# Optimization experiments

Measured on AMD Instinct MI355X. Metric: run time of the kernel, lower is better.

The kernel has to match this reference:

```python
import jax, jax.numpy as jnp
import numpy as np

H, HKV, D = 16, 4, 64
ROPE_BASE = 10000.0
EPS = 1e-6


def _rms_norm(x):
    return x * jax.lax.rsqrt(jnp.mean(x * x, axis=-1, keepdims=True) + EPS)


def _rope_cos_sin(T, dtype):
    inv_freq = 1.0 / (ROPE_BASE ** (jnp.arange(0, D, 2, dtype=jnp.float32) / D))  # [D/2]
    t = jnp.arange(T, dtype=jnp.float32)
    freqs = jnp.outer(t, inv_freq)  # [T, D/2]
    return jnp.cos(freqs)[None, :, None, :].astype(dtype), jnp.sin(freqs)[None, :, None, :].astype(dtype)


def _apply_rope(x, cos, sin):
    d = x.shape[-1] // 2
    x1, x2 = x[..., :d], x[..., d:]
    return jnp.concatenate([x1 * cos + x2 * sin, -x1 * sin + x2 * cos], axis=-1)


def setup_inputs() -> dict:
    key = jax.random.key(0)
    ks = jax.random.split(key, 6)
    B, T, dm = 1, 2048, 1024
    x = jax.random.normal(ks[0], (B, T, dm), dtype=jnp.float32)
    q_w = jax.random.normal(ks[1], (H * D, dm), dtype=jnp.float32) * 0.02
    k_w = jax.random.normal(ks[2], (HKV * D, dm), dtype=jnp.float32) * 0.02
    v_w = jax.random.normal(ks[3], (HKV * D, dm), dtype=jnp.float32) * 0.02
    o_w = jax.random.normal(ks[4], (dm, H * D), dtype=jnp.float32) * 0.02
    temp = jnp.ones((H,), dtype=jnp.float32) * np.sqrt(D)  # per-head temperature buffer
    curvature = jnp.asarray(1.0, dtype=jnp.float32)
    return {"x": x, "q_w": q_w, "k_w": k_w, "v_w": v_w, "o_w": o_w, "temp": temp, "curvature": curvature}


def reference(x, q_w, k_w, v_w, o_w, temp, curvature):
    B, T, dm = x.shape
    # projections
    q = (x @ q_w.T).reshape(B, T, H, D)
    k = (x @ k_w.T).reshape(B, T, HKV, D)
    v = (x @ v_w.T).reshape(B, T, HKV, D)
    q, k = _rms_norm(q), _rms_norm(k)
    cos, sin = _rope_cos_sin(T, q.dtype)
    q = _apply_rope(q, cos, sin)
    k = _apply_rope(k, cos, sin)
    # GQA: repeat kv heads
    rep = H // HKV
    k = jnp.repeat(k, rep, axis=2)  # [B,T,H,D]
    v = jnp.repeat(v, rep, axis=2)
    c = curvature
    # hyperboloid lift: time component x0 = sqrt(1/c + ||x||^2)
    q0 = jnp.sqrt(1.0 / c + jnp.sum(q * q, axis=-1))  # [B,T,H]
    k0 = jnp.sqrt(1.0 / c + jnp.sum(k * k, axis=-1))
    # Minkowski inner product <q,k>_L = q.k_spatial - q0*k0  -> [B,H,Tq,Tk]
    mink = jnp.einsum('bqhd,bkhd->bhqk', q, k) - q0.transpose(0, 2, 1)[..., :, None] * k0.transpose(0, 2, 1)[..., None, :]
    # Lorentz distance d = arccosh(clamp(-c*<q,k>_L, 1+eps)) / sqrt(c)
    dist = jnp.arccosh(jnp.maximum(-c * mink, 1.0 + 1e-5)) / jnp.sqrt(c)
    scores = -dist / temp[None, :, None, None]
    causal = jnp.tril(jnp.ones((T, T), dtype=bool))
    scores = jnp.where(causal[None, None], scores, -jnp.inf)
    w = jax.nn.softmax(scores, axis=-1)  # [B,H,Tq,Tk]
    attn = jnp.einsum('bhqk,bkhd->bqhd', w, v).reshape(B, T, H * D)
    out = attn @ o_w.T  # [B,T,dm]
    spatial_norm = jnp.mean(jnp.sqrt(jnp.sum(q * q, axis=-1)))
    return out, spatial_norm
```

## Files before the change

kernel.cpp:

```cpp
#include <hip/hip_runtime.h>
#include <hip/hip_bf16.h>

typedef __attribute__((ext_vector_type(8))) short short8;
typedef __attribute__((ext_vector_type(4))) short bf16x4;
typedef __attribute__((ext_vector_type(4))) float f32x4;

#define TT 2048
#define DM 1024
#define NH 16
#define NKV 4
#define HD 64

#define MFMA32(a,b,c) __builtin_amdgcn_mfma_f32_16x16x32_bf16(a,b,c,0,0,0)
#define MFMA16(a,b,c) __builtin_amdgcn_mfma_f32_16x16x16bf16_1k(a,b,c,0,0,0)

__device__ __forceinline__ unsigned short f2bf(float x){
  unsigned int u = __float_as_uint(x);
  u += 0x7fffu + ((u >> 16) & 1u);
  return (unsigned short)(u >> 16);
}
__device__ __forceinline__ unsigned int pkbf2(float x, float y){
  union { __hip_bfloat162 h; unsigned int u; } t;
  t.h = __float22bfloat162_rn(make_float2(x, y));
  return t.u;
}
__device__ __forceinline__ void gl_lds16(const unsigned short* g, unsigned short* l){
  __builtin_amdgcn_global_load_lds(
      (__attribute__((address_space(1))) void*)g,
      (__attribute__((address_space(3))) void*)l, 16, 0, 0);
}

__global__ __launch_bounds__(256) void convertw_kernel(
    const float* __restrict__ x,
    const float* __restrict__ qw, const float* __restrict__ kw,
    const float* __restrict__ vw, const float* __restrict__ ow,
    unsigned short* __restrict__ xb,
    unsigned short* __restrict__ wqkv, unsigned short* __restrict__ owb){
  long v = (long)blockIdx.x * 256 + threadIdx.x;
  const float* src; unsigned short* dst; long base;
  if      (v < 524288) { src = x;  dst = xb;             base = v; }
  else if (v < 786432) { src = qw; dst = wqkv;           base = v - 524288; }
  else if (v < 851968) { src = kw; dst = wqkv + 1048576; base = v - 786432; }
  else if (v < 917504) { src = vw; dst = wqkv + 1310720; base = v - 851968; }
  else                 { src = ow; dst = owb;            base = v - 917504; }
  f32x4 d = *(const f32x4*)(src + base * 4);
  uint2 pk = { pkbf2(d[0], d[1]), pkbf2(d[2], d[3]) };
  *(uint2*)(dst + base * 4) = pk;
}

__global__ __launch_bounds__(256) void gemm1_fused(
    const unsigned short* __restrict__ xb, const unsigned short* __restrict__ wqkv,
    unsigned short* __restrict__ qb, unsigned short* __restrict__ kb,
    unsigned short* __restrict__ vt,
    float* __restrict__ q0, float* __restrict__ k0,
    float* __restrict__ bpart, const float* __restrict__ curv){
  __shared__ __align__(16) unsigned short As[4 * 128 * 32];
  __shared__ __align__(16) unsigned short Bs[4 * 64 * 32];
  __shared__ float bsum;
  const int tid = threadIdx.x, lane = tid & 63, wave = tid >> 6;
  const int hIdx = blockIdx.x;
  const int bm = blockIdx.y * 128, bn = hIdx * 64;
  const int ml = lane & 15, quad = lane >> 4;
  if (tid == 0) bsum = 0.f;
  f32x4 acc[2][4];
  const f32x4 z = {0.f, 0.f, 0.f, 0.f};
#pragma unroll
  for (int i = 0; i < 2; i++)
#pragma unroll
    for (int j = 0; j < 4; j++) acc[i][j] = z;

  const int srow = tid >> 2, scol = (tid & 3) * 8;
  const unsigned short* Ag0 = xb   + (long)(bm + srow) * 1024 + scol;
  const unsigned short* Ag1 = Ag0 + 64 * 1024;
  const unsigned short* Bg  = wqkv + (long)(bn + srow) * 1024 + scol;

  for (int kk = 0; kk < 1024; kk += 128){
    __syncthreads();
#pragma unroll
    for (int half = 0; half < 4; half++){
      gl_lds16(Ag0 + kk + half * 32, As + half * 4096 + wave * 512);
      gl_lds16(Ag1 + kk + half * 32, As + half * 4096 + 2048 + wave * 512);
      gl_lds16(Bg  + kk + half * 32, Bs + half * 2048 + wave * 512);
    }
    __syncthreads();
#pragma unroll
    for (int half = 0; half < 4; half++){
      const unsigned short* Ah = As + half * 4096;
      const unsigned short* Bh = Bs + half * 2048;
      short8 a0 = *(const short8*)&Ah[(wave * 32 + ml) * 32 + quad * 8];
      short8 a1 = *(const short8*)&Ah[(wave * 32 + 16 + ml) * 32 + quad * 8];
      short8 b0 = *(const short8*)&Bh[(ml) * 32 + quad * 8];
      short8 b1 = *(const short8*)&Bh[(16 + ml) * 32 + quad * 8];
      short8 b2 = *(const short8*)&Bh[(32 + ml) * 32 + quad * 8];
      short8 b3 = *(const short8*)&Bh[(48 + ml) * 32 + quad * 8];
      acc[0][0] = MFMA32(a0, b0, acc[0][0]);
      acc[0][1] = MFMA32(a0, b1, acc[0][1]);
      acc[0][2] = MFMA32(a0, b2, acc[0][2]);
      acc[0][3] = MFMA32(a0, b3, acc[0][3]);
      acc[1][0] = MFMA32(a1, b0, acc[1][0]);
      acc[1][1] = MFMA32(a1, b1, acc[1][1]);
      acc[1][2] = MFMA32(a1, b2, acc[1][2]);
      acc[1][3] = MFMA32(a1, b3, acc[1][3]);
    }
  }

  if (hIdx < 20){
    const bool isq = hIdx < 16;
    const int h = isq ? hIdx : hIdx - 16;
    const float c = curv[0];
    unsigned short* ob = isq ? qb : kb;
    float* o0p = isq ? q0 : k0;
    const float if0 = __builtin_amdgcn_exp2f((float)ml        * (-13.287712379549449f / 32.f));
    const float if1 = __builtin_amdgcn_exp2f((float)(16 + ml) * (-13.287712379549449f / 32.f));
    float bl = 0.f;
#pragma unroll
    for (int i = 0; i < 2; i++){
#pragma unroll
      for (int r = 0; r < 4; r++){
        const int t = bm + wave * 32 + i * 16 + quad * 4 + r;
        float v0 = acc[i][0][r], v1 = acc[i][1][r], v2 = acc[i][2][r], v3 = acc[i][3][r];
        float ss = v0 * v0 + v1 * v1 + v2 * v2 + v3 * v3;
        ss += __shfl_xor(ss, 1); ss += __shfl_xor(ss, 2);
        ss += __shfl_xor(ss, 4); ss += __shfl_xor(ss, 8);
        float scale = __builtin_amdgcn_rsqf(ss * (1.f / 64.f) + 1e-6f);
        float x0 = v0 * scale, x1 = v1 * scale, x2 = v2 * scale, x3 = v3 * scale;
        float sn0, cs0, sn1, cs1;
        __sincosf((float)t * if0, &sn0, &cs0);
        __sincosf((float)t * if1, &sn1, &cs1);
        unsigned short* op = ob + ((long)h * TT + t) * 64;
        op[ml]      = f2bf( x0 * cs0 + x2 * sn0);
        op[16 + ml] = f2bf( x1 * cs1 + x3 * sn1);
        op[32 + ml] = f2bf( x2 * cs0 - x0 * sn0);
        op[48 + ml] = f2bf( x3 * cs1 - x1 * sn1);
        if (ml == 0){
          float sq = ss * scale * scale;
          o0p[h * TT + t] = __builtin_amdgcn_sqrtf(1.f / c + sq);
          if (isq) bl += __builtin_amdgcn_sqrtf(sq);
        }
      }
    }
    if (isq && ml == 0) atomicAdd(&bsum, bl);
  } else {
    const int hk = hIdx - 20;
#pragma unroll
    for (int i = 0; i < 2; i++){
      const int tile = (bm >> 4) + wave * 2 + i;
#pragma unroll
      for (int j = 0; j < 4; j++){
        uint2 w2 = { pkbf2(acc[i][j][0], acc[i][j][1]), pkbf2(acc[i][j][2], acc[i][j][3]) };
        unsigned short* dst = vt + ((long)(hk * 128 + tile) * 64 + j * 16 + ml) * 16 + quad * 4;
        *(uint2*)dst = w2;
      }
    }
  }
  __syncthreads();
  if (tid == 0) bpart[blockIdx.y * 24 + hIdx] = bsum;
}

__global__ __launch_bounds__(256, 3) void attn_kernel(
    const unsigned short* __restrict__ qb_, const unsigned short* __restrict__ kb_,
    const unsigned short* __restrict__ vt_,
    const float* __restrict__ q0_, const float* __restrict__ k0_,
    const float* __restrict__ temp, const float* __restrict__ curv,
    unsigned short* __restrict__ attn_out,
    const float* __restrict__ bpart, float* __restrict__ out_scalar){
  __shared__ float lds[8 * 1104];
  const int tid = threadIdx.x, lane = tid & 63, wave = tid >> 6;
  const int qt  = 127 - (blockIdx.x >> 3);
  const int sub = blockIdx.x & 7;
  const int kvh = sub >> 1, hp = sub & 1;
  const int h0 = kvh * 4 + hp * 2, h1 = h0 + 1;
  const int i0 = qt * 16;
  const int ml = lane & 15, quad = lane >> 4;
  const float c = curv[0];
  const float rsc = __builtin_amdgcn_rsqf(c);
  const float fac0 = -rsc / temp[h0];
  const float fac1 = -rsc / temp[h1];
  const f32x4 z = {0.f, 0.f, 0.f, 0.f};
  const unsigned short* kh = kb_ + (long)kvh * TT * 64;
  const unsigned short* vh = vt_ + (long)kvh * 128 * 1024;
  const float* k0h = k0_ + kvh * TT;

  short8 qa0 = *(const short8*)&qb_[((long)h0 * TT + i0 + ml) * 64 + quad * 8];
  short8 qa1 = *(const short8*)&qb_[((long)h0 * TT + i0 + ml) * 64 + 32 + quad * 8];
  short8 qb0 = *(const short8*)&qb_[((long)h1 * TT + i0 + ml) * 64 + quad * 8];
  short8 qb1 = *(const short8*)&qb_[((long)h1 * TT + i0 + ml) * 64 + 32 + quad * 8];
  const float q0c0 = c * q0_[h0 * TT + i0 + ml];
  const float q0c1 = c * q0_[h1 * TT + i0 + ml];
  const int rowq = i0 + ml;

  f32x4 o0[4], o1[4];
#pragma unroll
  for (int dt = 0; dt < 4; dt++){ o0[dt] = z; o1[dt] = z; }
  float l0 = 0.f, l1 = 0.f;

  const int nt = (i0 + 47) >> 5;

#pragma unroll 1
  for (int t = wave; t < nt; t += 4){
    const int j0 = t << 5;
    const unsigned short* kp = kh + (long)j0 * 64;
    short8 ka0 = *(const short8*)(kp + ml * 64 + quad * 8);
    short8 ka1 = *(const short8*)(kp + ml * 64 + 32 + quad * 8);
    short8 kc0 = *(const short8*)(kp + (16 + ml) * 64 + quad * 8);
    short8 kc1 = *(const short8*)(kp + (16 + ml) * 64 + 32 + quad * 8);
    f32x4 k0a = *(const f32x4*)(k0h + j0 + quad * 4);
    f32x4 k0b = *(const f32x4*)(k0h + j0 + 16 + quad * 4);
    const unsigned short* vpa = vh + (long)(j0 >> 4) * 1024;
    bf16x4 vfa0 = *(const bf16x4*)(vpa + ( 0 + ml) * 16 + quad * 4);
    bf16x4 vfa1 = *(const bf16x4*)(vpa + (16 + ml) * 16 + quad * 4);
    bf16x4 vfa2 = *(const bf16x4*)(vpa + (32 + ml) * 16 + quad * 4);
    bf16x4 vfa3 = *(const bf16x4*)(vpa + (48 + ml) * 16 + quad * 4);
    bf16x4 vfb0 = *(const bf16x4*)(vpa + 1024 + ( 0 + ml) * 16 + quad * 4);
    bf16x4 vfb1 = *(const bf16x4*)(vpa + 1024 + (16 + ml) * 16 + quad * 4);
    bf16x4 vfb2 = *(const bf16x4*)(vpa + 1024 + (32 + ml) * 16 + quad * 4);
    bf16x4 vfb3 = *(const bf16x4*)(vpa + 1024 + (48 + ml) * 16 + quad * 4);

    const int keyb = j0 + quad * 4;
    const bool nm = (j0 + 31 > i0);
    {
      f32x4 s0 = z, s1 = z;
      s0 = MFMA32(ka0, qa0, s0);
      s0 = MFMA32(ka1, qa1, s0);
      s1 = MFMA32(kc0, qa0, s1);
      s1 = MFMA32(kc1, qa1, s1);
      float p0[4], p1[4];
#pragma unroll
      for (int r = 0; r < 4; r++){
        float argA = fmaxf(__builtin_fmaf(-c, s0[r], q0c0 * k0a[r]), 1.00001f);
        float wA   = argA + __builtin_amdgcn_sqrtf(__builtin_fmaf(argA, argA, -1.f));
        float pA   = __builtin_amdgcn_exp2f(fac0 * __builtin_amdgcn_logf(wA));
        float argB = fmaxf(__builtin_fmaf(-c, s1[r], q0c0 * k0b[r]), 1.00001f);
        float wB   = argB + __builtin_amdgcn_sqrtf(__builtin_fmaf(argB, argB, -1.f));
        float pB   = __builtin_amdgcn_exp2f(fac0 * __builtin_amdgcn_logf(wB));
        if (nm){
          if (keyb + r > rowq)      pA = 0.f;
          if (keyb + 16 + r > rowq) pB = 0.f;
        }
        p0[r] = pA; p1[r] = pB;
        l0 += pA + pB;
      }
      uint2 pua = { pkbf2(p0[0], p0[1]), pkbf2(p0[2], p0[3]) };
      uint2 pub = { pkbf2(p1[0], p1[1]), pkbf2(p1[2], p1[3]) };
      bf16x4 pfa = *(bf16x4*)&pua;
      bf16x4 pfb = *(bf16x4*)&pub;
      o0[0] = MFMA16(vfa0, pfa, o0[0]);
      o0[1] = MFMA16(vfa1, pfa, o0[1]);
      o0[2] = MFMA16(vfa2, pfa, o0[2]);
      o0[3] = MFMA16(vfa3, pfa, o0[3]);
      o0[0] = MFMA16(vfb0, pfb, o0[0]);
      o0[1] = MFMA16(vfb1, pfb, o0[1]);
      o0[2] = MFMA16(vfb2, pfb, o0[2]);
      o0[3] = MFMA16(vfb3, pfb, o0[3]);
    }
    {
      f32x4 s0 = z, s1 = z;
      s0 = MFMA32(ka0, qb0, s0);
      s0 = MFMA32(ka1, qb1, s0);
      s1 = MFMA32(kc0, qb0, s1);
      s1 = MFMA32(kc1, qb1, s1);
      float p0[4], p1[4];
#pragma unroll
      for (int r = 0; r < 4; r++){
        float argA = fmaxf(__builtin_fmaf(-c, s0[r], q0c1 * k0a[r]), 1.00001f);
        float wA   = argA + __builtin_amdgcn_sqrtf(__builtin_fmaf(argA, argA, -1.f));
        float pA   = __builtin_amdgcn_exp2f(fac1 * __builtin_amdgcn_logf(wA));
        float argB = fmaxf(__builtin_fmaf(-c, s1[r], q0c1 * k0b[r]), 1.00001f);
        float wB   = argB + __builtin_amdgcn_sqrtf(__builtin_fmaf(argB, argB, -1.f));
        float pB   = __builtin_amdgcn_exp2f(fac1 * __builtin_amdgcn_logf(wB));
        if (nm){
          if (keyb + r > rowq)      pA = 0.f;
          if (keyb + 16 + r > rowq) pB = 0.f;
        }
        p0[r] = pA; p1[r] = pB;
        l1 += pA + pB;
      }
      uint2 pua = { pkbf2(p0[0], p0[1]), pkbf2(p0[2], p0[3]) };
      uint2 pub = { pkbf2(p1[0], p1[1]), pkbf2(p1[2], p1[3]) };
      bf16x4 pfa = *(bf16x4*)&pua;
      bf16x4 pfb = *(bf16x4*)&pub;
      o1[0] = MFMA16(vfa0, pfa, o1[0]);
      o1[1] = MFMA16(vfa1, pfa, o1[1]);
      o1[2] = MFMA16(vfa2, pfa, o1[2]);
      o1[3] = MFMA16(vfa3, pfa, o1[3]);
      o1[0] = MFMA16(vfb0, pfb, o1[0]);
      o1[1] = MFMA16(vfb1, pfb, o1[1]);
      o1[2] = MFMA16(vfb2, pfb, o1[2]);
      o1[3] = MFMA16(vfb3, pfb, o1[3]);
    }
  }
  l0 += __shfl_xor(l0, 16); l0 += __shfl_xor(l0, 32);
  l1 += __shfl_xor(l1, 16); l1 += __shfl_xor(l1, 32);
  {
    float* w0 = lds + wave * 1104;
    float* w1 = lds + (4 + wave) * 1104;
#pragma unroll
    for (int dt = 0; dt < 4; dt++){
      *(f32x4*)&w0[ml * 68 + dt * 16 + quad * 4] = o0[dt];
      *(f32x4*)&w1[ml * 68 + dt * 16 + quad * 4] = o1[dt];
    }
    if (quad == 0){ w0[1088 + ml] = l0; w1[1088 + ml] = l1; }
  }
  __syncthreads();
  {
    const int row = tid >> 4, c0 = (tid & 15) * 4;
#pragma unroll 1
    for (int hb = 0; hb < 2; hb++){
      const float* base = lds + hb * 4 * 1104;
      float L = 0.f; f32x4 s = z;
#pragma unroll
      for (int w = 0; w < 4; w++){
        const float* rg = base + w * 1104;
        L += rg[1088 + row];
        f32x4 t2 = *(const f32x4*)&rg[row * 68 + c0];
        s[0] += t2[0]; s[1] += t2[1]; s[2] += t2[2]; s[3] += t2[3];
      }
      float invL = __builtin_amdgcn_rcpf(L);
      const int h = hb ? h1 : h0;
      uint2 o = { pkbf2(s[0] * invL, s[1] * invL), pkbf2(s[2] * invL, s[3] * invL) };
      *(uint2*)&attn_out[(long)(i0 + row) * 1024 + h * 64 + c0] = o;
    }
  }
  if (blockIdx.x == 0 && tid < 64){
    float s = 0.f;
    for (int i = lane; i < 384; i += 64) s += bpart[i];
#pragma unroll
    for (int off = 1; off < 64; off <<= 1) s += __shfl_xor(s, off);
    if (lane == 0) out_scalar[0] = s * (1.f / 32768.f);
  }
}

__global__ __launch_bounds__(256) void gemm2_kernel(
    const unsigned short* __restrict__ A, const unsigned short* __restrict__ B,
    float* __restrict__ C){
  __shared__ __align__(16) unsigned short As[2 * 8192];
  __shared__ __align__(16) unsigned short Bs[2 * 4096];
  const int tid = threadIdx.x, lane = tid & 63, wave = tid >> 6;
  const int bm = blockIdx.y * 128, bn = blockIdx.x * 64;
  const int ml = lane & 15, quad = lane >> 4;
  f32x4 acc[2][4];
  const f32x4 z = {0.f, 0.f, 0.f, 0.f};
#pragma unroll
  for (int i = 0; i < 2; i++)
#pragma unroll
    for (int j = 0; j < 4; j++) acc[i][j] = z;

  const int srow = tid >> 2, scol = (tid & 3) * 8;
  const unsigned short* Ag0 = A + (long)(bm + srow) * 1024 + scol;
  const unsigned short* Ag1 = Ag0 + 64 * 1024;
  const unsigned short* Bg  = B + (long)(bn + srow) * 1024 + scol;

#define G2_STAGE(nb, ko)                                                  \
  do {                                                                    \
    gl_lds16(Ag0 + (ko),      As + (nb) * 8192 + wave * 512);             \
    gl_lds16(Ag1 + (ko),      As + (nb) * 8192 + 2048 + wave * 512);      \
    gl_lds16(Ag0 + (ko) + 32, As + (nb) * 8192 + 4096 + wave * 512);      \
    gl_lds16(Ag1 + (ko) + 32, As + (nb) * 8192 + 4096 + 2048 + wave * 512);\
    gl_lds16(Bg  + (ko),      Bs + (nb) * 4096 + wave * 512);             \
    gl_lds16(Bg  + (ko) + 32, Bs + (nb) * 4096 + 2048 + wave * 512);      \
  } while (0)

#define G2_COMPUTE(b)                                                     \
  do {                                                                    \
    _Pragma("unroll")                                                     \
    for (int half = 0; half < 2; half++){                                 \
      const unsigned short* Ah = As + (b) * 8192 + half * 4096;           \
      const unsigned short* Bh = Bs + (b) * 4096 + half * 2048;           \
      short8 a0 = *(const short8*)&Ah[(wave * 32 + ml) * 32 + quad * 8];  \
      short8 a1 = *(const short8*)&Ah[(wave * 32 + 16 + ml) * 32 + quad * 8];\
      short8 b0 = *(const short8*)&Bh[(ml) * 32 + quad * 8];              \
      short8 b1 = *(const short8*)&Bh[(16 + ml) * 32 + quad * 8];         \
      short8 b2 = *(const short8*)&Bh[(32 + ml) * 32 + quad * 8];         \
      short8 b3 = *(const short8*)&Bh[(48 + ml) * 32 + quad * 8];         \
      acc[0][0] = MFMA32(a0, b0, acc[0][0]);                              \
      acc[0][1] = MFMA32(a0, b1, acc[0][1]);                              \
      acc[0][2] = MFMA32(a0, b2, acc[0][2]);                              \
      acc[0][3] = MFMA32(a0, b3, acc[0][3]);                              \
      acc[1][0] = MFMA32(a1, b0, acc[1][0]);                              \
      acc[1][1] = MFMA32(a1, b1, acc[1][1]);                              \
      acc[1][2] = MFMA32(a1, b2, acc[1][2]);                              \
      acc[1][3] = MFMA32(a1, b3, acc[1][3]);                              \
    }                                                                     \
  } while (0)

  G2_STAGE(0, 0);
  __syncthreads();
  for (int kk = 0; kk < 1024; kk += 128){
    G2_STAGE(1, kk + 64);
    G2_COMPUTE(0);
    __syncthreads();
    if (kk + 128 < 1024) G2_STAGE(0, kk + 128);
    G2_COMPUTE(1);
    __syncthreads();
  }
#undef G2_STAGE
#undef G2_COMPUTE

#pragma unroll
  for (int i = 0; i < 2; i++)
#pragma unroll
    for (int j = 0; j < 4; j++)
#pragma unroll
      for (int r = 0; r < 4; r++)
        C[(long)(bm + wave * 32 + i * 16 + quad * 4 + r) * 1024 + bn + j * 16 + ml] = acc[i][j][r];
}

extern "C" void kernel_launch(void* const* d_in, const int* in_sizes, int n_in,
                              void* d_out, int out_size, void* d_ws, size_t ws_size,
                              hipStream_t stream){
  const float* x    = (const float*)d_in[0];
  const float* qw   = (const float*)d_in[1];
  const float* kw   = (const float*)d_in[2];
  const float* vw   = (const float*)d_in[3];
  const float* ow   = (const float*)d_in[4];
  const float* temp = (const float*)d_in[5];
  const float* curv = (const float*)d_in[6];
  float* out = (float*)d_out;

  char* ws = (char*)d_ws;
  size_t off = 0;
  auto alloc = [&](size_t bytes) -> char* {
    char* p = ws + off;
    off += (bytes + 255) & ~(size_t)255;
    return p;
  };
  unsigned short* xb   = (unsigned short*)alloc((size_t)TT * DM * 2);
  unsigned short* wqkv = (unsigned short*)alloc((size_t)1536 * DM * 2);
  unsigned short* owb  = (unsigned short*)alloc((size_t)DM * DM * 2);
  unsigned short* qb   = (unsigned short*)alloc((size_t)NH * TT * HD * 2);
  unsigned short* kb   = (unsigned short*)alloc((size_t)NKV * TT * HD * 2);
  unsigned short* vt   = (unsigned short*)alloc((size_t)NKV * TT * HD * 2);
  float*          q0   = (float*)alloc((size_t)NH * TT * 4);
  float*          k0   = (float*)alloc((size_t)NKV * TT * 4);
  unsigned short* attn = (unsigned short*)alloc((size_t)TT * DM * 2);
  float*          bpart= (float*)alloc((size_t)768 * 4);

  convertw_kernel<<<4608, 256, 0, stream>>>(x, qw, kw, vw, ow, xb, wqkv, owb);
  gemm1_fused<<<dim3(24, 16), 256, 0, stream>>>(xb, wqkv, qb, kb, vt, q0, k0, bpart, curv);
  attn_kernel<<<1024, 256, 0, stream>>>(qb, kb, vt, q0, k0, temp, curv, attn,
                                        bpart, out + (size_t)TT * DM);
  gemm2_kernel<<<dim3(16, 16), 256, 0, stream>>>(attn, owb, out);
}
```

Before: 140.3 us.

## Double query tile per attention block to reuse K/V loads across 32 rows

The attention kernel now processes 32 query rows per block instead of 16, with each wave computing four head/row-half combinations per key tile. Each loaded K and V fragment is therefore reused twice as often, cutting global/L2 traffic for K/V, and the grid is halved to 512 blocks. In exchange, register pressure roughly doubles, so launch bounds drop from 3 to 2 blocks per SM. Fewer blocks and coarser causal granularity may also worsen load balance and add wasted masked work on the diagonal tiles.

```diff
diff --git a/kernel.cpp b/kernel.cpp
--- a/kernel.cpp
+++ b/kernel.cpp
@@ -157,7 +157,44 @@
   if (tid == 0) bpart[blockIdx.y * 24 + hIdx] = bsum;
 }
 
-__global__ __launch_bounds__(256, 3) void attn_kernel(
+#define ATTN_STEP(QLO, QHI, Q0C, FAC, RQ, NM, OA, LACC)                         \
+  do {                                                                          \
+    f32x4 s0 = z, s1 = z;                                                       \
+    s0 = MFMA32(ka0, QLO, s0);                                                  \
+    s0 = MFMA32(ka1, QHI, s0);                                                  \
+    s1 = MFMA32(kc0, QLO, s1);                                                  \
+    s1 = MFMA32(kc1, QHI, s1);                                                  \
+    float p0[4], p1[4];                                                         \
+    _Pragma("unroll")                                                           \
+    for (int r = 0; r < 4; r++){                                                \
+      float argA = fmaxf(__builtin_fmaf(-c, s0[r], (Q0C) * k0a[r]), 1.00001f);  \
+      float wA   = argA + __builtin_amdgcn_sqrtf(__builtin_fmaf(argA, argA, -1.f)); \
+      float pA   = __builtin_amdgcn_exp2f((FAC) * __builtin_amdgcn_logf(wA));   \
+      float argB = fmaxf(__builtin_fmaf(-c, s1[r], (Q0C) * k0b[r]), 1.00001f);  \
+      float wB   = argB + __builtin_amdgcn_sqrtf(__builtin_fmaf(argB, argB, -1.f)); \
+      float pB   = __builtin_amdgcn_exp2f((FAC) * __builtin_amdgcn_logf(wB));   \
+      if (NM){                                                                  \
+        if (keyb + r > (RQ))      pA = 0.f;                                     \
+        if (keyb + 16 + r > (RQ)) pB = 0.f;                                     \
+      }                                                                         \
+      p0[r] = pA; p1[r] = pB;                                                   \
+      LACC += pA + pB;                                                          \
+    }                                                                           \
+    uint2 pua = { pkbf2(p0[0], p0[1]), pkbf2(p0[2], p0[3]) };                   \
+    uint2 pub = { pkbf2(p1[0], p1[1]), pkbf2(p1[2], p1[3]) };                   \
+    bf16x4 pfa = *(bf16x4*)&pua;                                                \
+    bf16x4 pfb = *(bf16x4*)&pub;                                                \
+    OA[0] = MFMA16(vfa0, pfa, OA[0]);                                           \
+    OA[1] = MFMA16(vfa1, pfa, OA[1]);                                           \
+    OA[2] = MFMA16(vfa2, pfa, OA[2]);                                           \
+    OA[3] = MFMA16(vfa3, pfa, OA[3]);                                           \
+    OA[0] = MFMA16(vfb0, pfb, OA[0]);                                           \
+    OA[1] = MFMA16(vfb1, pfb, OA[1]);                                           \
+    OA[2] = MFMA16(vfb2, pfb, OA[2]);                                           \
+    OA[3] = MFMA16(vfb3, pfb, OA[3]);                                           \
+  } while (0)
+
+__global__ __launch_bounds__(256, 2) void attn_kernel(
     const unsigned short* __restrict__ qb_, const unsigned short* __restrict__ kb_,
     const unsigned short* __restrict__ vt_,
     const float* __restrict__ q0_, const float* __restrict__ k0_,
@@ -166,11 +203,11 @@
     const float* __restrict__ bpart, float* __restrict__ out_scalar){
   __shared__ float lds[8 * 1104];
   const int tid = threadIdx.x, lane = tid & 63, wave = tid >> 6;
-  const int qt  = 127 - (blockIdx.x >> 3);
+  const int qt  = 63 - (blockIdx.x >> 3);
   const int sub = blockIdx.x & 7;
   const int kvh = sub >> 1, hp = sub & 1;
   const int h0 = kvh * 4 + hp * 2, h1 = h0 + 1;
-  const int i0 = qt * 16;
+  const int i0 = qt * 32;
   const int ml = lane & 15, quad = lane >> 4;
   const float c = curv[0];
   const float rsc = __builtin_amdgcn_rsqf(c);
@@ -181,20 +218,26 @@
   const unsigned short* vh = vt_ + (long)kvh * 128 * 1024;
   const float* k0h = k0_ + kvh * TT;
 
-  short8 qa0 = *(const short8*)&qb_[((long)h0 * TT + i0 + ml) * 64 + quad * 8];
-  short8 qa1 = *(const short8*)&qb_[((long)h0 * TT + i0 + ml) * 64 + 32 + quad * 8];
-  short8 qb0 = *(const short8*)&qb_[((long)h1 * TT + i0 + ml) * 64 + quad * 8];
-  short8 qb1 = *(const short8*)&qb_[((long)h1 * TT + i0 + ml) * 64 + 32 + quad * 8];
-  const float q0c0 = c * q0_[h0 * TT + i0 + ml];
-  const float q0c1 = c * q0_[h1 * TT + i0 + ml];
-  const int rowq = i0 + ml;
-
-  f32x4 o0[4], o1[4];
-#pragma unroll
-  for (int dt = 0; dt < 4; dt++){ o0[dt] = z; o1[dt] = z; }
-  float l0 = 0.f, l1 = 0.f;
-
-  const int nt = (i0 + 47) >> 5;
+  short8 qa00 = *(const short8*)&qb_[((long)h0 * TT + i0 + ml) * 64 + quad * 8];
+  short8 qa01 = *(const short8*)&qb_[((long)h0 * TT + i0 + ml) * 64 + 32 + quad * 8];
+  short8 qa10 = *(const short8*)&qb_[((long)h0 * TT + i0 + 16 + ml) * 64 + quad * 8];
+  short8 qa11 = *(const short8*)&qb_[((long)h0 * TT + i0 + 16 + ml) * 64 + 32 + quad * 8];
+  short8 qb00 = *(const short8*)&qb_[((long)h1 * TT + i0 + ml) * 64 + quad * 8];
+  short8 qb01 = *(const short8*)&qb_[((long)h1 * TT + i0 + ml) * 64 + 32 + quad * 8];
+  short8 qb10 = *(const short8*)&qb_[((long)h1 * TT + i0 + 16 + ml) * 64 + quad * 8];
+  short8 qb11 = *(const short8*)&qb_[((long)h1 * TT + i0 + 16 + ml) * 64 + 32 + quad * 8];
+  const float q0c0a = c * q0_[h0 * TT + i0 + ml];
+  const float q0c0b = c * q0_[h0 * TT + i0 + 16 + ml];
+  const float q0c1a = c * q0_[h1 * TT + i0 + ml];
+  const float q0c1b = c * q0_[h1 * TT + i0 + 16 + ml];
+  const int rqa = i0 + ml, rqb = i0 + 16 + ml;
+
+  f32x4 o0a[4], o0b[4], o1a[4], o1b[4];
+#pragma unroll
+  for (int dt = 0; dt < 4; dt++){ o0a[dt] = z; o0b[dt] = z; o1a[dt] = z; o1b[dt] = z; }
+  float l0a = 0.f, l0b = 0.f, l1a = 0.f, l1b = 0.f;
+
+  const int nt = (i0 + 63) >> 5;
 
 #pragma unroll 1
   for (int t = wave; t < nt; t += 4){
@@ -217,109 +260,55 @@
     bf16x4 vfb3 = *(const bf16x4*)(vpa + 1024 + (48 + ml) * 16 + quad * 4);
 
     const int keyb = j0 + quad * 4;
-    const bool nm = (j0 + 31 > i0);
+    const bool nma = (j0 + 31 > i0);
+    const bool nmb = (j0 + 31 > i0 + 16);
+
+    ATTN_STEP(qa00, qa01, q0c0a, fac0, rqa, nma, o0a, l0a);
+    ATTN_STEP(qa10, qa11, q0c0b, fac0, rqb, nmb, o0b, l0b);
+    ATTN_STEP(qb00, qb01, q0c1a, fac1, rqa, nma, o1a, l1a);
+    ATTN_STEP(qb10, qb11, q0c1b, fac1, rqb, nmb, o1b, l1b);
+  }
+  l0a += __shfl_xor(l0a, 16); l0a += __shfl_xor(l0a, 32);
+  l0b += __shfl_xor(l0b, 16); l0b += __shfl_xor(l0b, 32);
+  l1a += __shfl_xor(l1a, 16); l1a += __shfl_xor(l1a, 32);
+  l1b += __shfl_xor(l1b, 16); l1b += __shfl_xor(l1b, 32);
+
+#pragma unroll 1
+  for (int qs = 0; qs < 2; qs++){
     {
-      f32x4 s0 = z, s1 = z;
-      s0 = MFMA32(ka0, qa0, s0);
-      s0 = MFMA32(ka1, qa1, s0);
-      s1 = MFMA32(kc0, qa0, s1);
-      s1 = MFMA32(kc1, qa1, s1);
-      float p0[4], p1[4];
-#pragma unroll
-      for (int r = 0; r < 4; r++){
-        float argA = fmaxf(__builtin_fmaf(-c, s0[r], q0c0 * k0a[r]), 1.00001f);
-        float wA   = argA + __builtin_amdgcn_sqrtf(__builtin_fmaf(argA, argA, -1.f));
-        float pA   = __builtin_amdgcn_exp2f(fac0 * __builtin_amdgcn_logf(wA));
-        float argB = fmaxf(__builtin_fmaf(-c, s1[r], q0c0 * k0b[r]), 1.00001f);
-        float wB   = argB + __builtin_amdgcn_sqrtf(__builtin_fmaf(argB, argB, -1.f));
-        float pB   = __builtin_amdgcn_exp2f(fac0 * __builtin_amdgcn_logf(wB));
-        if (nm){
-          if (keyb + r > rowq)      pA = 0.f;
-          if (keyb + 16 + r > rowq) pB = 0.f;
+      float* w0 = lds + wave * 1104;
+      float* w1 = lds + (4 + wave) * 1104;
+#pragma unroll
+      for (int dt = 0; dt < 4; dt++){
+        *(f32x4*)&w0[ml * 68 + dt * 16 + quad * 4] = qs ? o0b[dt] : o0a[dt];
+        *(f32x4*)&w1[ml * 68 + dt * 16 + quad * 4] = qs ? o1b[dt] : o1a[dt];
+      }
+      if (quad == 0){
+        w0[1088 + ml] = qs ? l0b : l0a;
+        w1[1088 + ml] = qs ? l1b : l1a;
+      }
+    }
+    __syncthreads();
+    {
+      const int row = tid >> 4, c0 = (tid & 15) * 4;
+#pragma unroll 1
+      for (int hb = 0; hb < 2; hb++){
+        const float* base = lds + hb * 4 * 1104;
+        float L = 0.f; f32x4 s = z;
+#pragma unroll
+        for (int w = 0; w < 4; w++){
+          const float* rg = base + w * 1104;
+          L += rg[1088 + row];
+          f32x4 t2 = *(const f32x4*)&rg[row * 68 + c0];
+          s[0] += t2[0]; s[1] += t2[1]; s[2] += t2[2]; s[3] += t2[3];
         }
-        p0[r] = pA; p1[r] = pB;
-        l0 += pA + pB;
+        float invL = __builtin_amdgcn_rcpf(L);
+        const int h = hb ? h1 : h0;
+        uint2 o = { pkbf2(s[0] * invL, s[1] * invL), pkbf2(s[2] * invL, s[3] * invL) };
+        *(uint2*)&attn_out[(long)(i0 + qs * 16 + row) * 1024 + h * 64 + c0] = o;
       }
-      uint2 pua = { pkbf2(p0[0], p0[1]), pkbf2(p0[2], p0[3]) };
-      uint2 pub = { pkbf2(p1[0], p1[1]), pkbf2(p1[2], p1[3]) };
-      bf16x4 pfa = *(bf16x4*)&pua;
-      bf16x4 pfb = *(bf16x4*)&pub;
-      o0[0] = MFMA16(vfa0, pfa, o0[0]);
-      o0[1] = MFMA16(vfa1, pfa, o0[1]);
-      o0[2] = MFMA16(vfa2, pfa, o0[2]);
-      o0[3] = MFMA16(vfa3, pfa, o0[3]);
-      o0[0] = MFMA16(vfb0, pfb, o0[0]);
-      o0[1] = MFMA16(vfb1, pfb, o0[1]);
-      o0[2] = MFMA16(vfb2, pfb, o0[2]);
-      o0[3] = MFMA16(vfb3, pfb, o0[3]);
-    }
-    {
-      f32x4 s0 = z, s1 = z;
-      s0 = MFMA32(ka0, qb0, s0);
-      s0 = MFMA32(ka1, qb1, s0);
-      s1 = MFMA32(kc0, qb0, s1);
-      s1 = MFMA32(kc1, qb1, s1);
-      float p0[4], p1[4];
-#pragma unroll
-      for (int r = 0; r < 4; r++){
-        float argA = fmaxf(__builtin_fmaf(-c, s0[r], q0c1 * k0a[r]), 1.00001f);
-        float wA   = argA + __builtin_amdgcn_sqrtf(__builtin_fmaf(argA, argA, -1.f));
-        float pA   = __builtin_amdgcn_exp2f(fac1 * __builtin_amdgcn_logf(wA));
-        float argB = fmaxf(__builtin_fmaf(-c, s1[r], q0c1 * k0b[r]), 1.00001f);
-        float wB   = argB + __builtin_amdgcn_sqrtf(__builtin_fmaf(argB, argB, -1.f));
-        float pB   = __builtin_amdgcn_exp2f(fac1 * __builtin_amdgcn_logf(wB));
-        if (nm){
-          if (keyb + r > rowq)      pA = 0.f;
-          if (keyb + 16 + r > rowq) pB = 0.f;
-        }
-        p0[r] = pA; p1[r] = pB;
-        l1 += pA + pB;
-      }
-      uint2 pua = { pkbf2(p0[0], p0[1]), pkbf2(p0[2], p0[3]) };
-      uint2 pub = { pkbf2(p1[0], p1[1]), pkbf2(p1[2], p1[3]) };
-      bf16x4 pfa = *(bf16x4*)&pua;
-      bf16x4 pfb = *(bf16x4*)&pub;
-      o1[0] = MFMA16(vfa0, pfa, o1[0]);
-      o1[1] = MFMA16(vfa1, pfa, o1[1]);
-      o1[2] = MFMA16(vfa2, pfa, o1[2]);
-      o1[3] = MFMA16(vfa3, pfa, o1[3]);
-      o1[0] = MFMA16(vfb0, pfb, o1[0]);
-      o1[1] = MFMA16(vfb1, pfb, o1[1]);
-      o1[2] = MFMA16(vfb2, pfb, o1[2]);
-      o1[3] = MFMA16(vfb3, pfb, o1[3]);
-    }
-  }
-  l0 += __shfl_xor(l0, 16); l0 += __shfl_xor(l0, 32);
-  l1 += __shfl_xor(l1, 16); l1 += __shfl_xor(l1, 32);
-  {
-    float* w0 = lds + wave * 1104;
-    float* w1 = lds + (4 + wave) * 1104;
-#pragma unroll
-    for (int dt = 0; dt < 4; dt++){
-      *(f32x4*)&w0[ml * 68 + dt * 16 + quad * 4] = o0[dt];
-      *(f32x4*)&w1[ml * 68 + dt * 16 + quad * 4] = o1[dt];
-    }
-    if (quad == 0){ w0[1088 + ml] = l0; w1[1088 + ml] = l1; }
-  }
-  __syncthreads();
-  {
-    const int row = tid >> 4, c0 = (tid & 15) * 4;
-#pragma unroll 1
-    for (int hb = 0; hb < 2; hb++){
-      const float* base = lds + hb * 4 * 1104;
-      float L = 0.f; f32x4 s = z;
-#pragma unroll
-      for (int w = 0; w < 4; w++){
-        const float* rg = base + w * 1104;
-        L += rg[1088 + row];
-        f32x4 t2 = *(const f32x4*)&rg[row * 68 + c0];
-        s[0] += t2[0]; s[1] += t2[1]; s[2] += t2[2]; s[3] += t2[3];
-      }
-      float invL = __builtin_amdgcn_rcpf(L);
-      const int h = hb ? h1 : h0;
-      uint2 o = { pkbf2(s[0] * invL, s[1] * invL), pkbf2(s[2] * invL, s[3] * invL) };
-      *(uint2*)&attn_out[(long)(i0 + row) * 1024 + h * 64 + c0] = o;
-    }
+    }
+    __syncthreads();
   }
   if (blockIdx.x == 0 && tid < 64){
     float s = 0.f;
@@ -437,7 +426,7 @@
 
   convertw_kernel<<<4608, 256, 0, stream>>>(x, qw, kw, vw, ow, xb, wqkv, owb);
   gemm1_fused<<<dim3(24, 16), 256, 0, stream>>>(xb, wqkv, qb, kb, vt, q0, k0, bpart, curv);
-  attn_kernel<<<1024, 256, 0, stream>>>(qb, kb, vt, q0, k0, temp, curv, attn,
-                                        bpart, out + (size_t)TT * DM);
+  attn_kernel<<<512, 256, 0, stream>>>(qb, kb, vt, q0, k0, temp, curv, attn,
+                                       bpart, out + (size_t)TT * DM);
   gemm2_kernel<<<dim3(16, 16), 256, 0, stream>>>(attn, owb, out);
 }
```

Result: no change. 140.7 us (+0.3%).
